# Performance work log

Hardware: AMD Instinct MI355X
Metric: run time of the kernel (lower is better)

Reference implementation:

```python
import jax, jax.numpy as jnp
import numpy as np

D_MODEL = 1024
N_HEADS = 16
HEAD_DIM = D_MODEL // N_HEADS


def setup_inputs() -> dict:
    key = jax.random.key(0)
    k1, k2, k3, k4, k5 = jax.random.split(key, 5)
    B, S = 2, 2048
    x = jax.random.normal(k1, (B, S, D_MODEL), dtype=jnp.float32)
    mask = jnp.ones((B, 1, S), dtype=jnp.int32)
    s1 = 1.0 / np.sqrt(D_MODEL)
    qkv_w = jax.random.normal(k2, (3 * D_MODEL, D_MODEL), dtype=jnp.float32) * s1
    qkv_b = jax.random.normal(k3, (3 * D_MODEL,), dtype=jnp.float32) * 0.02
    wo_w = jax.random.normal(k4, (D_MODEL, D_MODEL), dtype=jnp.float32) * s1
    wo_b = jax.random.normal(k5, (D_MODEL,), dtype=jnp.float32) * 0.02
    return {"x": x, "mask": mask, "qkv_w": qkv_w, "qkv_b": qkv_b, "wo_w": wo_w, "wo_b": wo_b}


def reference(x, mask, qkv_w, qkv_b, wo_w, wo_b):
    B, S, _ = x.shape
    # fused QKV projection: [B,S,3d]
    qkv = jnp.einsum('bsd,ed->bse', x, qkv_w) + qkv_b
    qkv = qkv.reshape(B, S, 3, N_HEADS, HEAD_DIM).transpose(2, 0, 3, 1, 4)
    q, k, v = qkv[0], qkv[1], qkv[2]  # each [B,H,S,hd]
    scores = jnp.einsum('bhsd,bhtd->bhst', q, k) / np.sqrt(HEAD_DIM)
    # mask [B,1,S] -> [B,1,1,S]; fill -inf where mask == 0
    scores = jnp.where(mask[:, None] == 0, -jnp.inf, scores)
    weights = jax.nn.softmax(scores, axis=-1)  # dropout p=0.0 -> identity
    out = jnp.einsum('bhst,bhtd->bhsd', weights, v)
    out = out.transpose(0, 2, 1, 3).reshape(B, S, D_MODEL)
    out = jnp.einsum('bsd,ed->bse', out, wo_w) + wo_b
    return out, weights
```

## Files before the change

### kernel.cpp

```cpp
#include <hip/hip_runtime.h>
#include <cstdint>
#include <cstddef>

typedef unsigned short u16;
typedef __attribute__((ext_vector_type(8))) short bf16x8;
typedef __attribute__((ext_vector_type(4))) float f32x4;

#define DEV static __device__ __forceinline__

DEV void gload_lds16(const void* g, void* l) {
  __builtin_amdgcn_global_load_lds((const __attribute__((address_space(1))) void*)g,
                                   (__attribute__((address_space(3))) void*)l, 16, 0, 0);
}

DEV u16 f2bf(float f) {
  unsigned x = __float_as_uint(f);
  return (u16)((x + 0x7FFFu + ((x >> 16) & 1u)) >> 16);
}

DEV unsigned cvtpk(float lo, float hi) {
  unsigned r;
  asm("v_cvt_pk_bf16_f32 %0, %1, %2" : "=v"(r) : "v"(lo), "v"(hi));
  return r;
}

#if __has_builtin(__builtin_amdgcn_exp2f)
DEV float fexp2(float x) { return __builtin_amdgcn_exp2f(x); }
#else
DEV float fexp2(float x) { return exp2f(x); }
#endif

#define WAITV(n)                                                   \
  do {                                                             \
    asm volatile("s_waitcnt vmcnt(" #n ")" ::: "memory");          \
    __builtin_amdgcn_sched_barrier(0);                             \
  } while (0)

DEV void sbar() {
  __builtin_amdgcn_sched_barrier(0);
  __builtin_amdgcn_s_barrier();
  __builtin_amdgcn_sched_barrier(0);
}

__global__ __launch_bounds__(256) void cvt3(const float* __restrict__ a, u16* __restrict__ da,
                                            const float* __restrict__ b, u16* __restrict__ db,
                                            const float* __restrict__ c, u16* __restrict__ dc) {
  int bid = blockIdx.x;
  const float* s;
  u16* d;
  int base;
  if (bid < 4096) { s = a; d = da; base = bid; }
  else if (bid < 7168) { s = b; d = db; base = bid - 4096; }
  else { s = c; d = dc; base = bid - 7168; }
  const int i = (base * 256 + (int)threadIdx.x) * 4;
  float4 v = *(const float4*)(s + i);
  uint2 p;
  p.x = (unsigned)f2bf(v.x) | ((unsigned)f2bf(v.y) << 16);
  p.y = (unsigned)f2bf(v.z) | ((unsigned)f2bf(v.w) << 16);
  *(uint2*)(d + i) = p;
}

template <int EPI, int BM, int BN>
__global__ __launch_bounds__(256) void gemm_bt(const u16* __restrict__ A,
                                               const u16* __restrict__ Bm,
                                               const float* __restrict__ bias,
                                               void* __restrict__ Cout,
                                               u16* __restrict__ Vt,
                                               int M, int N, int K) {
  __shared__ u16 As[2][BM * 32];
  __shared__ u16 Bs[2][BN * 32];
  constexpr int MT = BM / 32, NT = BN / 32;
  const int cpx = (int)gridDim.x >> 3;
  const int bid = ((int)blockIdx.x & 7) * cpx + ((int)blockIdx.x >> 3);
  const int nb = N / BN;
  const int m0 = (bid / nb) * BM;
  const int n0 = (bid % nb) * BN;
  const int tid = threadIdx.x;
  const int w = tid >> 6, lane = tid & 63;
  const int wm = (w >> 1) * (BM / 2), wn = (w & 1) * (BN / 2);
  const int lr = lane & 15, lg = lane >> 4;

  f32x4 acc[MT][NT];
  const f32x4 z4 = {0.f, 0.f, 0.f, 0.f};
#pragma unroll
  for (int m = 0; m < MT; ++m)
#pragma unroll
    for (int n = 0; n < NT; ++n) acc[m][n] = z4;

  auto stage = [&](int ks, int buf) {
    const int k0 = ks << 5;
#pragma unroll
    for (int i = 0; i < BM * 4 / 256; ++i) {
      const int o = i * 256 + tid;
      const int row = o >> 2, c = o & 3;
      gload_lds16(A + (size_t)(m0 + row) * K + k0 + c * 8, &As[buf][(i * 256 + w * 64) * 8]);
    }
#pragma unroll
    for (int i = 0; i < BN * 4 / 256; ++i) {
      const int o = i * 256 + tid;
      const int row = o >> 2, c = o & 3;
      gload_lds16(Bm + (size_t)(n0 + row) * K + k0 + c * 8, &Bs[buf][(i * 256 + w * 64) * 8]);
    }
  };

  const int nk = K >> 5;
  stage(0, 0);
  __syncthreads();
  for (int ks = 0; ks < nk; ++ks) {
    const int cur = ks & 1;
    if (ks + 1 < nk) stage(ks + 1, cur ^ 1);
    bf16x8 af[MT], bfr[NT];
#pragma unroll
    for (int m = 0; m < MT; ++m)
      af[m] = *(const bf16x8*)&As[cur][(wm + m * 16 + lr) * 32 + lg * 8];
#pragma unroll
    for (int n = 0; n < NT; ++n)
      bfr[n] = *(const bf16x8*)&Bs[cur][(wn + n * 16 + lr) * 32 + lg * 8];
    __builtin_amdgcn_s_setprio(1);
#pragma unroll
    for (int m = 0; m < MT; ++m)
#pragma unroll
      for (int n = 0; n < NT; ++n)
        acc[m][n] = __builtin_amdgcn_mfma_f32_16x16x32_bf16(af[m], bfr[n], acc[m][n], 0, 0, 0);
    __builtin_amdgcn_s_setprio(0);
    __syncthreads();
  }

#pragma unroll
  for (int n = 0; n < NT; ++n) {
    const int e = n0 + wn + n * 16 + lr;
    const float bv = bias[e];
    if (EPI == 1 && (e >> 10) == 2) {
      const int h = (e >> 6) & 15, d = e & 63;
#pragma unroll
      for (int m = 0; m < MT; ++m) {
        const int row0 = m0 + wm + m * 16 + lg * 4;
        const int bb = row0 >> 11, s0 = row0 & 2047;
        uint2 pv;
        pv.x = cvtpk(acc[m][n][0] + bv, acc[m][n][1] + bv);
        pv.y = cvtpk(acc[m][n][2] + bv, acc[m][n][3] + bv);
        *(uint2*)(Vt + (size_t)(bb * 16 + h) * 131072 + (size_t)d * 2048 + s0) = pv;
      }
    } else {
#pragma unroll
      for (int m = 0; m < MT; ++m) {
#pragma unroll
        for (int r = 0; r < 4; ++r) {
          const int row = m0 + wm + m * 16 + lg * 4 + r;
          const float v = acc[m][n][r] + bv;
          if (EPI == 0) {
            ((float*)Cout)[(size_t)row * N + e] = v;
          } else {
            const int which = e >> 10, h = (e >> 6) & 15, d = e & 63;
            const int bb = row >> 11, s = row & 2047;
            ((u16*)Cout)[(size_t)which * 4194304 +
                         (((size_t)(bb * 16 + h) * 2048 + s) << 6) + d] = f2bf(v);
          }
        }
      }
    }
  }
}

__global__ __launch_bounds__(256, 4) void attn(const u16* __restrict__ Q,
                                               const u16* __restrict__ Kg,
                                               const u16* __restrict__ Vtg,
                                               const int* __restrict__ mask,
                                               float* __restrict__ Wout,
                                               u16* __restrict__ Og) {
  __shared__ u16 Ks[2][64 * 64];
  __shared__ u16 Vs[2][64 * 64];
  __shared__ u16 Pl[4][16 * 64];
  const int L = ((int)blockIdx.x & 7) * 128 + ((int)blockIdx.x >> 3);
  const int bh = L >> 5, qt = L & 31;
  const int b = bh >> 4, h = bh & 15;
  const int tid = threadIdx.x;
  const int w = tid >> 6, lane = tid & 63;
  const int lr = lane & 15, lg = lane >> 4;
  const int srow0 = qt * 64 + w * 16;
  const float C2 = 0.18033688011112042f;
  const float M2 = 11.541560327111707f;

  const u16* qrow = Q + ((size_t)bh * 2048 + srow0 + lr) * 64;
  const bf16x8 qf0 = *(const bf16x8*)(qrow + lg * 8);
  const bf16x8 qf1 = *(const bf16x8*)(qrow + 32 + lg * 8);
  const int* mrow = mask + b * 2048;

  auto stageK = [&](int kt, u16* dst) {
    const u16* g = Kg + (size_t)bh * 131072 + (size_t)kt * 4096;
#pragma unroll
    for (int iss = 0; iss < 2; ++iss) {
      const int o = iss * 256 + tid;
      const int row = o >> 3, c = o & 7;
      gload_lds16(g + row * 64 + ((c ^ (row & 7)) << 3), dst + (iss * 256 + w * 64) * 8);
    }
  };
  auto stageV = [&](int kt, u16* dst) {
    const u16* g = Vtg + (size_t)bh * 131072 + kt * 64;
#pragma unroll
    for (int iss = 0; iss < 2; ++iss) {
      const int o = iss * 256 + tid;
      const int row = o >> 3, c = o & 7;
      gload_lds16(g + (size_t)row * 2048 + ((c ^ (row & 7)) << 3),
                  dst + (iss * 256 + w * 64) * 8);
    }
  };
  auto probs = [&](const u16* kb, int kt, f32x4* pr) {
    int4 mv[4];
#pragma unroll
    for (int n = 0; n < 4; ++n) mv[n] = *(const int4*)&mrow[kt * 64 + n * 16 + lg * 4];
    f32x4 sc[4];
    __builtin_amdgcn_s_setprio(1);
#pragma unroll
    for (int n = 0; n < 4; ++n) {
      const int tr = n * 16 + lr;
      const bf16x8 k0 = *(const bf16x8*)&kb[tr * 64 + ((lg ^ (tr & 7)) << 3)];
      const bf16x8 k1 = *(const bf16x8*)&kb[tr * 64 + (((lg + 4) ^ (tr & 7)) << 3)];
      f32x4 s = {0.f, 0.f, 0.f, 0.f};
      s = __builtin_amdgcn_mfma_f32_16x16x32_bf16(k0, qf0, s, 0, 0, 0);
      s = __builtin_amdgcn_mfma_f32_16x16x32_bf16(k1, qf1, s, 0, 0, 0);
      sc[n] = s;
    }
    __builtin_amdgcn_s_setprio(0);
#pragma unroll
    for (int n = 0; n < 4; ++n) {
      f32x4 p;
      p[0] = (mv[n].x == 0) ? 0.f : fexp2(fmaf(sc[n][0], C2, -M2));
      p[1] = (mv[n].y == 0) ? 0.f : fexp2(fmaf(sc[n][1], C2, -M2));
      p[2] = (mv[n].z == 0) ? 0.f : fexp2(fmaf(sc[n][2], C2, -M2));
      p[3] = (mv[n].w == 0) ? 0.f : fexp2(fmaf(sc[n][3], C2, -M2));
      pr[n] = p;
    }
  };

  stageK(0, &Ks[0][0]);
  stageK(1, &Ks[1][0]);
  WAITV(2);
  sbar();
  float lsum = 0.f;
  int cur3 = 0, stg3 = 2;
  for (int t = 0; t < 32; ++t) {
    u16* curb = (cur3 == 0) ? &Ks[0][0] : ((cur3 == 1) ? &Ks[1][0] : &Vs[0][0]);
    if (t + 2 < 32) {
      u16* stb = (stg3 == 0) ? &Ks[0][0] : ((stg3 == 1) ? &Ks[1][0] : &Vs[0][0]);
      stageK(t + 2, stb);
    }
    f32x4 pr[4];
    probs(curb, t, pr);
    float s0 = (pr[0][0] + pr[0][1]) + (pr[0][2] + pr[0][3]);
    float s1 = (pr[1][0] + pr[1][1]) + (pr[1][2] + pr[1][3]);
    float s2 = (pr[2][0] + pr[2][1]) + (pr[2][2] + pr[2][3]);
    float s3 = (pr[3][0] + pr[3][1]) + (pr[3][2] + pr[3][3]);
    lsum += (s0 + s1) + (s2 + s3);
    if (t + 1 < 32) {
      if (t + 2 < 32) {
        WAITV(6);
      } else {
        WAITV(0);
      }
      sbar();
    }
    cur3 = (cur3 == 2) ? 0 : cur3 + 1;
    stg3 = (stg3 == 2) ? 0 : stg3 + 1;
  }
  lsum += __shfl_xor(lsum, 16);
  lsum += __shfl_xor(lsum, 32);
  const float rl = 1.0f / lsum;

  sbar();
  f32x4 oacc[4];
  const f32x4 z4 = {0.f, 0.f, 0.f, 0.f};
#pragma unroll
  for (int n = 0; n < 4; ++n) oacc[n] = z4;

  float* wrow = Wout + ((size_t)bh * 2048 + srow0 + lr) * 2048;
  char* plw = (char*)&Pl[w][0];
  const int pswz = (lr & 7) << 4;

  stageK(0, &Ks[0][0]);
  stageV(0, &Vs[0][0]);
  WAITV(0);
  sbar();
  for (int t = 0; t < 32; ++t) {
    const int cur = t & 1;
    if (t + 1 < 32) {
      stageK(t + 1, &Ks[cur ^ 1][0]);
      stageV(t + 1, &Vs[cur ^ 1][0]);
    }
    f32x4 pr[4];
    probs(&Ks[cur][0], t, pr);
#pragma unroll
    for (int n = 0; n < 4; ++n) {
      f32x4 wv;
      wv[0] = pr[n][0] * rl;
      wv[1] = pr[n][1] * rl;
      wv[2] = pr[n][2] * rl;
      wv[3] = pr[n][3] * rl;
      __builtin_nontemporal_store(wv, (f32x4*)&wrow[t * 64 + n * 16 + lg * 4]);
      uint2 pw;
      pw.x = cvtpk(wv[0], wv[1]);
      pw.y = cvtpk(wv[2], wv[3]);
      *(uint2*)(plw + (lr * 128 + ((n * 32 + lg * 8) ^ pswz))) = pw;
    }
    const bf16x8 pf0 = *(const bf16x8*)(plw + (lr * 128 + ((lg * 16) ^ pswz)));
    const bf16x8 pf1 = *(const bf16x8*)(plw + (lr * 128 + ((64 + lg * 16) ^ pswz)));
    __builtin_amdgcn_s_setprio(1);
#pragma unroll
    for (int n = 0; n < 4; ++n) {
      const int dr = n * 16 + lr;
      const bf16x8 v0 = *(const bf16x8*)&Vs[cur][dr * 64 + ((lg ^ (dr & 7)) << 3)];
      const bf16x8 v1 = *(const bf16x8*)&Vs[cur][dr * 64 + (((lg + 4) ^ (dr & 7)) << 3)];
      oacc[n] = __builtin_amdgcn_mfma_f32_16x16x32_bf16(pf0, v0, oacc[n], 0, 0, 0);
      oacc[n] = __builtin_amdgcn_mfma_f32_16x16x32_bf16(pf1, v1, oacc[n], 0, 0, 0);
    }
    __builtin_amdgcn_s_setprio(0);
    if (t + 1 < 32) {
      WAITV(8);
      sbar();
    }
  }

#pragma unroll
  for (int n = 0; n < 4; ++n) {
#pragma unroll
    for (int r = 0; r < 4; ++r) {
      const int s = srow0 + lg * 4 + r;
      Og[((size_t)(b * 2048 + s)) * 1024 + h * 64 + n * 16 + lr] = f2bf(oacc[n][r]);
    }
  }
}

extern "C" void kernel_launch(void* const* d_in, const int* in_sizes, int n_in,
                              void* d_out, int out_size, void* d_ws, size_t ws_size,
                              hipStream_t stream) {
  const float* x     = (const float*)d_in[0];
  const int*   mask  = (const int*)d_in[1];
  const float* qkv_w = (const float*)d_in[2];
  const float* qkv_b = (const float*)d_in[3];
  const float* wo_w  = (const float*)d_in[4];
  const float* wo_b  = (const float*)d_in[5];
  float* out = (float*)d_out;

  char* ws = (char*)d_ws;
  u16* xb   = (u16*)(ws);
  u16* qwb  = (u16*)(ws + (8u << 20));
  u16* wob  = (u16*)(ws + (14u << 20));
  u16* qkvb = (u16*)(ws + (16u << 20));
  u16* vt   = (u16*)(ws + (40u << 20));
  u16* ob   = (u16*)(ws + (48u << 20));

  cvt3<<<8192, 256, 0, stream>>>(x, xb, qkv_w, qwb, wo_w, wob);
  gemm_bt<1, 128, 128><<<768, 256, 0, stream>>>(xb, qwb, qkv_b, qkvb, vt, 4096, 3072, 1024);
  attn<<<1024, 256, 0, stream>>>(qkvb, qkvb + 4194304, vt, mask, out + 4194304, ob);
  gemm_bt<0, 128, 64><<<512, 256, 0, stream>>>(ob, wob, wo_b, out, nullptr, 4096, 1024, 1024);
}
```

Baseline: 248.2 us.

## Process two query tiles per attention block to reuse K/V LDS tiles

Each attention block now handles 128 query rows: every wave computes two 16-row query subtiles against each staged K/V tile, so K and V are loaded into LDS half as often. The first pass stages 128-row K chunks in one larger double buffer. The grid is halved, launch bounds go to 2 blocks per CU, and the wait counts are adjusted for the extra loads. The cost is higher register pressure and fewer resident blocks. The kernel is likely dominated by writing the large fp32 weights output, so the reuse gain may be small.

```diff
diff --git a/kernel.cpp b/kernel.cpp
--- a/kernel.cpp
+++ b/kernel.cpp
@@ -162,30 +162,41 @@
   }
 }
 
-__global__ __launch_bounds__(256, 4) void attn(const u16* __restrict__ Q,
+__global__ __launch_bounds__(256, 2) void attn(const u16* __restrict__ Q,
                                                const u16* __restrict__ Kg,
                                                const u16* __restrict__ Vtg,
                                                const int* __restrict__ mask,
                                                float* __restrict__ Wout,
                                                u16* __restrict__ Og) {
-  __shared__ u16 Ks[2][64 * 64];
-  __shared__ u16 Vs[2][64 * 64];
-  __shared__ u16 Pl[4][16 * 64];
-  const int L = ((int)blockIdx.x & 7) * 128 + ((int)blockIdx.x >> 3);
-  const int bh = L >> 5, qt = L & 31;
+  __shared__ u16 SM[2][8192];
+  __shared__ u16 Pl[4][2][1024];
+  const int L = ((int)blockIdx.x & 7) * 64 + ((int)blockIdx.x >> 3);
+  const int bh = L >> 4, qt = L & 15;
   const int b = bh >> 4, h = bh & 15;
   const int tid = threadIdx.x;
   const int w = tid >> 6, lane = tid & 63;
   const int lr = lane & 15, lg = lane >> 4;
-  const int srow0 = qt * 64 + w * 16;
+  const int srow0 = qt * 128 + w * 16;
   const float C2 = 0.18033688011112042f;
   const float M2 = 11.541560327111707f;
 
-  const u16* qrow = Q + ((size_t)bh * 2048 + srow0 + lr) * 64;
-  const bf16x8 qf0 = *(const bf16x8*)(qrow + lg * 8);
-  const bf16x8 qf1 = *(const bf16x8*)(qrow + 32 + lg * 8);
+  const u16* qr0 = Q + ((size_t)bh * 2048 + srow0 + lr) * 64;
+  const u16* qr1 = qr0 + 64 * 64;
+  const bf16x8 qf00 = *(const bf16x8*)(qr0 + lg * 8);
+  const bf16x8 qf01 = *(const bf16x8*)(qr0 + 32 + lg * 8);
+  const bf16x8 qf10 = *(const bf16x8*)(qr1 + lg * 8);
+  const bf16x8 qf11 = *(const bf16x8*)(qr1 + 32 + lg * 8);
   const int* mrow = mask + b * 2048;
 
+  auto stageChunk = [&](int ch, u16* dst) {
+    const u16* g = Kg + (size_t)bh * 131072 + (size_t)ch * 8192;
+#pragma unroll
+    for (int iss = 0; iss < 4; ++iss) {
+      const int o = iss * 256 + tid;
+      const int row = o >> 3, c = o & 7;
+      gload_lds16(g + row * 64 + ((c ^ (row & 7)) << 3), dst + (iss * 256 + w * 64) * 8);
+    }
+  };
   auto stageK = [&](int kt, u16* dst) {
     const u16* g = Kg + (size_t)bh * 131072 + (size_t)kt * 4096;
 #pragma unroll
@@ -205,129 +216,166 @@
                   dst + (iss * 256 + w * 64) * 8);
     }
   };
-  auto probs = [&](const u16* kb, int kt, f32x4* pr) {
+  auto probsT = [&](const u16* kb, int tt, int kt, f32x4 pr[2][4]) {
     int4 mv[4];
 #pragma unroll
     for (int n = 0; n < 4; ++n) mv[n] = *(const int4*)&mrow[kt * 64 + n * 16 + lg * 4];
-    f32x4 sc[4];
-    __builtin_amdgcn_s_setprio(1);
+    bf16x8 k0[4], k1[4];
 #pragma unroll
     for (int n = 0; n < 4; ++n) {
       const int tr = n * 16 + lr;
-      const bf16x8 k0 = *(const bf16x8*)&kb[tr * 64 + ((lg ^ (tr & 7)) << 3)];
-      const bf16x8 k1 = *(const bf16x8*)&kb[tr * 64 + (((lg + 4) ^ (tr & 7)) << 3)];
+      k0[n] = *(const bf16x8*)&kb[tt + tr * 64 + ((lg ^ (tr & 7)) << 3)];
+      k1[n] = *(const bf16x8*)&kb[tt + tr * 64 + (((lg + 4) ^ (tr & 7)) << 3)];
+    }
+    f32x4 sc[2][4];
+    __builtin_amdgcn_s_setprio(1);
+#pragma unroll
+    for (int n = 0; n < 4; ++n) {
       f32x4 s = {0.f, 0.f, 0.f, 0.f};
-      s = __builtin_amdgcn_mfma_f32_16x16x32_bf16(k0, qf0, s, 0, 0, 0);
-      s = __builtin_amdgcn_mfma_f32_16x16x32_bf16(k1, qf1, s, 0, 0, 0);
-      sc[n] = s;
+      s = __builtin_amdgcn_mfma_f32_16x16x32_bf16(k0[n], qf00, s, 0, 0, 0);
+      s = __builtin_amdgcn_mfma_f32_16x16x32_bf16(k1[n], qf01, s, 0, 0, 0);
+      sc[0][n] = s;
+      f32x4 s2 = {0.f, 0.f, 0.f, 0.f};
+      s2 = __builtin_amdgcn_mfma_f32_16x16x32_bf16(k0[n], qf10, s2, 0, 0, 0);
+      s2 = __builtin_amdgcn_mfma_f32_16x16x32_bf16(k1[n], qf11, s2, 0, 0, 0);
+      sc[1][n] = s2;
     }
     __builtin_amdgcn_s_setprio(0);
 #pragma unroll
-    for (int n = 0; n < 4; ++n) {
-      f32x4 p;
-      p[0] = (mv[n].x == 0) ? 0.f : fexp2(fmaf(sc[n][0], C2, -M2));
-      p[1] = (mv[n].y == 0) ? 0.f : fexp2(fmaf(sc[n][1], C2, -M2));
-      p[2] = (mv[n].z == 0) ? 0.f : fexp2(fmaf(sc[n][2], C2, -M2));
-      p[3] = (mv[n].w == 0) ? 0.f : fexp2(fmaf(sc[n][3], C2, -M2));
-      pr[n] = p;
-    }
+    for (int hh = 0; hh < 2; ++hh)
+#pragma unroll
+      for (int n = 0; n < 4; ++n) {
+        f32x4 p;
+        p[0] = (mv[n].x == 0) ? 0.f : fexp2(fmaf(sc[hh][n][0], C2, -M2));
+        p[1] = (mv[n].y == 0) ? 0.f : fexp2(fmaf(sc[hh][n][1], C2, -M2));
+        p[2] = (mv[n].z == 0) ? 0.f : fexp2(fmaf(sc[hh][n][2], C2, -M2));
+        p[3] = (mv[n].w == 0) ? 0.f : fexp2(fmaf(sc[hh][n][3], C2, -M2));
+        pr[hh][n] = p;
+      }
   };
 
-  stageK(0, &Ks[0][0]);
-  stageK(1, &Ks[1][0]);
-  WAITV(2);
+  float ls0 = 0.f, ls1 = 0.f;
+  stageChunk(0, &SM[0][0]);
+  WAITV(0);
   sbar();
-  float lsum = 0.f;
-  int cur3 = 0, stg3 = 2;
-  for (int t = 0; t < 32; ++t) {
-    u16* curb = (cur3 == 0) ? &Ks[0][0] : ((cur3 == 1) ? &Ks[1][0] : &Vs[0][0]);
-    if (t + 2 < 32) {
-      u16* stb = (stg3 == 0) ? &Ks[0][0] : ((stg3 == 1) ? &Ks[1][0] : &Vs[0][0]);
-      stageK(t + 2, stb);
-    }
-    f32x4 pr[4];
-    probs(curb, t, pr);
-    float s0 = (pr[0][0] + pr[0][1]) + (pr[0][2] + pr[0][3]);
-    float s1 = (pr[1][0] + pr[1][1]) + (pr[1][2] + pr[1][3]);
-    float s2 = (pr[2][0] + pr[2][1]) + (pr[2][2] + pr[2][3]);
-    float s3 = (pr[3][0] + pr[3][1]) + (pr[3][2] + pr[3][3]);
-    lsum += (s0 + s1) + (s2 + s3);
-    if (t + 1 < 32) {
-      if (t + 2 < 32) {
-        WAITV(6);
-      } else {
-        WAITV(0);
-      }
+  for (int r = 0; r < 16; ++r) {
+    const u16* cb = &SM[r & 1][0];
+    if (r + 1 < 16) stageChunk(r + 1, &SM[(r + 1) & 1][0]);
+#pragma unroll
+    for (int half = 0; half < 2; ++half) {
+      f32x4 pr[2][4];
+      probsT(cb, half * 4096, 2 * r + half, pr);
+      {
+        float s0 = (pr[0][0][0] + pr[0][0][1]) + (pr[0][0][2] + pr[0][0][3]);
+        float s1 = (pr[0][1][0] + pr[0][1][1]) + (pr[0][1][2] + pr[0][1][3]);
+        float s2 = (pr[0][2][0] + pr[0][2][1]) + (pr[0][2][2] + pr[0][2][3]);
+        float s3 = (pr[0][3][0] + pr[0][3][1]) + (pr[0][3][2] + pr[0][3][3]);
+        ls0 += (s0 + s1) + (s2 + s3);
+      }
+      {
+        float s0 = (pr[1][0][0] + pr[1][0][1]) + (pr[1][0][2] + pr[1][0][3]);
+        float s1 = (pr[1][1][0] + pr[1][1][1]) + (pr[1][1][2] + pr[1][1][3]);
+        float s2 = (pr[1][2][0] + pr[1][2][1]) + (pr[1][2][2] + pr[1][2][3]);
+        float s3 = (pr[1][3][0] + pr[1][3][1]) + (pr[1][3][2] + pr[1][3][3]);
+        ls1 += (s0 + s1) + (s2 + s3);
+      }
+    }
+    if (r + 1 < 16) {
+      WAITV(8);
       sbar();
     }
-    cur3 = (cur3 == 2) ? 0 : cur3 + 1;
-    stg3 = (stg3 == 2) ? 0 : stg3 + 1;
   }
-  lsum += __shfl_xor(lsum, 16);
-  lsum += __shfl_xor(lsum, 32);
-  const float rl = 1.0f / lsum;
+  ls0 += __shfl_xor(ls0, 16);
+  ls0 += __shfl_xor(ls0, 32);
+  ls1 += __shfl_xor(ls1, 16);
+  ls1 += __shfl_xor(ls1, 32);
+  const float rl0 = 1.0f / ls0, rl1 = 1.0f / ls1;
 
   sbar();
-  f32x4 oacc[4];
+  f32x4 oacc[2][4];
   const f32x4 z4 = {0.f, 0.f, 0.f, 0.f};
 #pragma unroll
-  for (int n = 0; n < 4; ++n) oacc[n] = z4;
-
-  float* wrow = Wout + ((size_t)bh * 2048 + srow0 + lr) * 2048;
-  char* plw = (char*)&Pl[w][0];
+  for (int hh = 0; hh < 2; ++hh)
+#pragma unroll
+    for (int n = 0; n < 4; ++n) oacc[hh][n] = z4;
+
+  float* wrow0 = Wout + ((size_t)bh * 2048 + srow0 + lr) * 2048;
+  float* wrow1 = wrow0 + (size_t)64 * 2048;
+  char* plw0 = (char*)&Pl[w][0][0];
+  char* plw1 = (char*)&Pl[w][1][0];
   const int pswz = (lr & 7) << 4;
 
-  stageK(0, &Ks[0][0]);
-  stageV(0, &Vs[0][0]);
+  stageK(0, &SM[0][0]);
+  stageV(0, &SM[1][0]);
   WAITV(0);
   sbar();
   for (int t = 0; t < 32; ++t) {
     const int cur = t & 1;
+    u16* kcur = &SM[0][cur * 4096];
+    u16* vcur = &SM[1][cur * 4096];
     if (t + 1 < 32) {
-      stageK(t + 1, &Ks[cur ^ 1][0]);
-      stageV(t + 1, &Vs[cur ^ 1][0]);
-    }
-    f32x4 pr[4];
-    probs(&Ks[cur][0], t, pr);
+      stageK(t + 1, &SM[0][(cur ^ 1) * 4096]);
+      stageV(t + 1, &SM[1][(cur ^ 1) * 4096]);
+    }
+    f32x4 pr[2][4];
+    probsT(kcur, 0, t, pr);
 #pragma unroll
     for (int n = 0; n < 4; ++n) {
       f32x4 wv;
-      wv[0] = pr[n][0] * rl;
-      wv[1] = pr[n][1] * rl;
-      wv[2] = pr[n][2] * rl;
-      wv[3] = pr[n][3] * rl;
-      __builtin_nontemporal_store(wv, (f32x4*)&wrow[t * 64 + n * 16 + lg * 4]);
+      wv[0] = pr[0][n][0] * rl0;
+      wv[1] = pr[0][n][1] * rl0;
+      wv[2] = pr[0][n][2] * rl0;
+      wv[3] = pr[0][n][3] * rl0;
+      __builtin_nontemporal_store(wv, (f32x4*)&wrow0[t * 64 + n * 16 + lg * 4]);
       uint2 pw;
       pw.x = cvtpk(wv[0], wv[1]);
       pw.y = cvtpk(wv[2], wv[3]);
-      *(uint2*)(plw + (lr * 128 + ((n * 32 + lg * 8) ^ pswz))) = pw;
-    }
-    const bf16x8 pf0 = *(const bf16x8*)(plw + (lr * 128 + ((lg * 16) ^ pswz)));
-    const bf16x8 pf1 = *(const bf16x8*)(plw + (lr * 128 + ((64 + lg * 16) ^ pswz)));
+      *(uint2*)(plw0 + (lr * 128 + ((n * 32 + lg * 8) ^ pswz))) = pw;
+    }
+#pragma unroll
+    for (int n = 0; n < 4; ++n) {
+      f32x4 wv;
+      wv[0] = pr[1][n][0] * rl1;
+      wv[1] = pr[1][n][1] * rl1;
+      wv[2] = pr[1][n][2] * rl1;
+      wv[3] = pr[1][n][3] * rl1;
+      __builtin_nontemporal_store(wv, (f32x4*)&wrow1[t * 64 + n * 16 + lg * 4]);
+      uint2 pw;
+      pw.x = cvtpk(wv[0], wv[1]);
+      pw.y = cvtpk(wv[2], wv[3]);
+      *(uint2*)(plw1 + (lr * 128 + ((n * 32 + lg * 8) ^ pswz))) = pw;
+    }
+    const bf16x8 pA0 = *(const bf16x8*)(plw0 + (lr * 128 + ((lg * 16) ^ pswz)));
+    const bf16x8 pA1 = *(const bf16x8*)(plw0 + (lr * 128 + ((64 + lg * 16) ^ pswz)));
+    const bf16x8 pB0 = *(const bf16x8*)(plw1 + (lr * 128 + ((lg * 16) ^ pswz)));
+    const bf16x8 pB1 = *(const bf16x8*)(plw1 + (lr * 128 + ((64 + lg * 16) ^ pswz)));
     __builtin_amdgcn_s_setprio(1);
 #pragma unroll
     for (int n = 0; n < 4; ++n) {
       const int dr = n * 16 + lr;
-      const bf16x8 v0 = *(const bf16x8*)&Vs[cur][dr * 64 + ((lg ^ (dr & 7)) << 3)];
-      const bf16x8 v1 = *(const bf16x8*)&Vs[cur][dr * 64 + (((lg + 4) ^ (dr & 7)) << 3)];
-      oacc[n] = __builtin_amdgcn_mfma_f32_16x16x32_bf16(pf0, v0, oacc[n], 0, 0, 0);
-      oacc[n] = __builtin_amdgcn_mfma_f32_16x16x32_bf16(pf1, v1, oacc[n], 0, 0, 0);
+      const bf16x8 v0 = *(const bf16x8*)&vcur[dr * 64 + ((lg ^ (dr & 7)) << 3)];
+      const bf16x8 v1 = *(const bf16x8*)&vcur[dr * 64 + (((lg + 4) ^ (dr & 7)) << 3)];
+      oacc[0][n] = __builtin_amdgcn_mfma_f32_16x16x32_bf16(pA0, v0, oacc[0][n], 0, 0, 0);
+      oacc[0][n] = __builtin_amdgcn_mfma_f32_16x16x32_bf16(pA1, v1, oacc[0][n], 0, 0, 0);
+      oacc[1][n] = __builtin_amdgcn_mfma_f32_16x16x32_bf16(pB0, v0, oacc[1][n], 0, 0, 0);
+      oacc[1][n] = __builtin_amdgcn_mfma_f32_16x16x32_bf16(pB1, v1, oacc[1][n], 0, 0, 0);
     }
     __builtin_amdgcn_s_setprio(0);
     if (t + 1 < 32) {
-      WAITV(8);
+      WAITV(12);
       sbar();
     }
   }
 
 #pragma unroll
-  for (int n = 0; n < 4; ++n) {
-#pragma unroll
-    for (int r = 0; r < 4; ++r) {
-      const int s = srow0 + lg * 4 + r;
-      Og[((size_t)(b * 2048 + s)) * 1024 + h * 64 + n * 16 + lr] = f2bf(oacc[n][r]);
-    }
-  }
+  for (int hh = 0; hh < 2; ++hh)
+#pragma unroll
+    for (int n = 0; n < 4; ++n)
+#pragma unroll
+      for (int r = 0; r < 4; ++r) {
+        const int s = srow0 + hh * 64 + lg * 4 + r;
+        Og[((size_t)(b * 2048 + s)) * 1024 + h * 64 + n * 16 + lr] = f2bf(oacc[hh][n][r]);
+      }
 }
 
 extern "C" void kernel_launch(void* const* d_in, const int* in_sizes, int n_in,
@@ -351,6 +399,6 @@
 
   cvt3<<<8192, 256, 0, stream>>>(x, xb, qkv_w, qwb, wo_w, wob);
   gemm_bt<1, 128, 128><<<768, 256, 0, stream>>>(xb, qwb, qkv_b, qkvb, vt, 4096, 3072, 1024);
-  attn<<<1024, 256, 0, stream>>>(qkvb, qkvb + 4194304, vt, mask, out + 4194304, ob);
+  attn<<<512, 256, 0, stream>>>(qkvb, qkvb + 4194304, vt, mask, out + 4194304, ob);
   gemm_bt<0, 128, 64><<<512, 256, 0, stream>>>(ob, wob, wo_b, out, nullptr, 4096, 1024, 1024);
 }
```

Result: slower. 276.6 us (+11.4%).

## Bit-pack mask and restage attention weights through LDS for coalesced stores

Applied to the files above, without the earlier changes.

The attention kernel now stages the normalized fp32 probabilities through a swizzled LDS tile per wave. Each group of 8 lanes then writes one contiguous 128-byte row segment of the large weights output, instead of 16-byte pieces scattered across 16 rows. The same LDS readback builds the bf16 P fragment for the PV MFMA, split into two K halves. The int32 mask is pre-packed into bitwords by an extra block in the conversion kernel. An all-ones check skips the per-element select work. The cost is extra LDS traffic and instructions per tile, plus a workspace region for the packed mask placed inside the qkv buffer area.

```diff
diff --git a/kernel.cpp b/kernel.cpp
--- a/kernel.cpp
+++ b/kernel.cpp
@@ -44,8 +44,20 @@
 
 __global__ __launch_bounds__(256) void cvt3(const float* __restrict__ a, u16* __restrict__ da,
                                             const float* __restrict__ b, u16* __restrict__ db,
-                                            const float* __restrict__ c, u16* __restrict__ dc) {
+                                            const float* __restrict__ c, u16* __restrict__ dc,
+                                            const int* __restrict__ mask,
+                                            unsigned* __restrict__ mpack) {
   int bid = blockIdx.x;
+  if (bid == 8192) {
+    const int j = threadIdx.x;
+    if (j < 128) {
+      const int* mb = mask + (j >> 6) * 2048 + (j & 63) * 32;
+      unsigned bits = 0;
+      for (int k = 0; k < 32; ++k) bits |= (mb[k] != 0 ? 1u : 0u) << k;
+      mpack[j] = bits;
+    }
+    return;
+  }
   const float* s;
   u16* d;
   int base;
@@ -165,12 +177,12 @@
 __global__ __launch_bounds__(256, 4) void attn(const u16* __restrict__ Q,
                                                const u16* __restrict__ Kg,
                                                const u16* __restrict__ Vtg,
-                                               const int* __restrict__ mask,
+                                               const unsigned* __restrict__ mpack,
                                                float* __restrict__ Wout,
                                                u16* __restrict__ Og) {
-  __shared__ u16 Ks[2][64 * 64];
-  __shared__ u16 Vs[2][64 * 64];
-  __shared__ u16 Pl[4][16 * 64];
+  __shared__ u16 Ks[2][4096];
+  __shared__ u16 Vs[2][4096];
+  __shared__ float Pf[4][512];
   const int L = ((int)blockIdx.x & 7) * 128 + ((int)blockIdx.x >> 3);
   const int bh = L >> 5, qt = L & 31;
   const int b = bh >> 4, h = bh & 15;
@@ -184,7 +196,7 @@
   const u16* qrow = Q + ((size_t)bh * 2048 + srow0 + lr) * 64;
   const bf16x8 qf0 = *(const bf16x8*)(qrow + lg * 8);
   const bf16x8 qf1 = *(const bf16x8*)(qrow + 32 + lg * 8);
-  const int* mrow = mask + b * 2048;
+  const unsigned* mpk = mpack + b * 64;
 
   auto stageK = [&](int kt, u16* dst) {
     const u16* g = Kg + (size_t)bh * 131072 + (size_t)kt * 4096;
@@ -205,32 +217,20 @@
                   dst + (iss * 256 + w * 64) * 8);
     }
   };
-  auto probs = [&](const u16* kb, int kt, f32x4* pr) {
-    int4 mv[4];
-#pragma unroll
-    for (int n = 0; n < 4; ++n) mv[n] = *(const int4*)&mrow[kt * 64 + n * 16 + lg * 4];
-    f32x4 sc[4];
+  auto qk = [&](const u16* kb, f32x4* sc) {
+    const f32x4 z4 = {0.f, 0.f, 0.f, 0.f};
     __builtin_amdgcn_s_setprio(1);
 #pragma unroll
     for (int n = 0; n < 4; ++n) {
       const int tr = n * 16 + lr;
       const bf16x8 k0 = *(const bf16x8*)&kb[tr * 64 + ((lg ^ (tr & 7)) << 3)];
       const bf16x8 k1 = *(const bf16x8*)&kb[tr * 64 + (((lg + 4) ^ (tr & 7)) << 3)];
-      f32x4 s = {0.f, 0.f, 0.f, 0.f};
+      f32x4 s = z4;
       s = __builtin_amdgcn_mfma_f32_16x16x32_bf16(k0, qf0, s, 0, 0, 0);
       s = __builtin_amdgcn_mfma_f32_16x16x32_bf16(k1, qf1, s, 0, 0, 0);
       sc[n] = s;
     }
     __builtin_amdgcn_s_setprio(0);
-#pragma unroll
-    for (int n = 0; n < 4; ++n) {
-      f32x4 p;
-      p[0] = (mv[n].x == 0) ? 0.f : fexp2(fmaf(sc[n][0], C2, -M2));
-      p[1] = (mv[n].y == 0) ? 0.f : fexp2(fmaf(sc[n][1], C2, -M2));
-      p[2] = (mv[n].z == 0) ? 0.f : fexp2(fmaf(sc[n][2], C2, -M2));
-      p[3] = (mv[n].w == 0) ? 0.f : fexp2(fmaf(sc[n][3], C2, -M2));
-      pr[n] = p;
-    }
   };
 
   stageK(0, &Ks[0][0]);
@@ -241,20 +241,34 @@
   int cur3 = 0, stg3 = 2;
   for (int t = 0; t < 32; ++t) {
     u16* curb = (cur3 == 0) ? &Ks[0][0] : ((cur3 == 1) ? &Ks[1][0] : &Vs[0][0]);
+    const unsigned mx = mpk[t * 2], my = mpk[t * 2 + 1];
     if (t + 2 < 32) {
       u16* stb = (stg3 == 0) ? &Ks[0][0] : ((stg3 == 1) ? &Ks[1][0] : &Vs[0][0]);
       stageK(t + 2, stb);
     }
-    f32x4 pr[4];
-    probs(curb, t, pr);
-    float s0 = (pr[0][0] + pr[0][1]) + (pr[0][2] + pr[0][3]);
-    float s1 = (pr[1][0] + pr[1][1]) + (pr[1][2] + pr[1][3]);
-    float s2 = (pr[2][0] + pr[2][1]) + (pr[2][2] + pr[2][3]);
-    float s3 = (pr[3][0] + pr[3][1]) + (pr[3][2] + pr[3][3]);
-    lsum += (s0 + s1) + (s2 + s3);
+    f32x4 sc[4];
+    qk(curb, sc);
+    f32x4 p[4];
+#pragma unroll
+    for (int n = 0; n < 4; ++n)
+#pragma unroll
+      for (int r = 0; r < 4; ++r) p[n][r] = fexp2(fmaf(sc[n][r], C2, -M2));
+    if ((mx & my) != 0xFFFFFFFFu) {
+#pragma unroll
+      for (int n = 0; n < 4; ++n) {
+        const unsigned wsel = (n < 2) ? mx : my;
+#pragma unroll
+        for (int r = 0; r < 4; ++r) {
+          const unsigned bit = (wsel >> ((n & 1) * 16 + lg * 4 + r)) & 1u;
+          p[n][r] = bit ? p[n][r] : 0.f;
+        }
+      }
+    }
+#pragma unroll
+    for (int n = 0; n < 4; ++n) lsum += (p[n][0] + p[n][1]) + (p[n][2] + p[n][3]);
     if (t + 1 < 32) {
       if (t + 2 < 32) {
-        WAITV(6);
+        WAITV(2);
       } else {
         WAITV(0);
       }
@@ -273,9 +287,10 @@
 #pragma unroll
   for (int n = 0; n < 4; ++n) oacc[n] = z4;
 
-  float* wrow = Wout + ((size_t)bh * 2048 + srow0 + lr) * 2048;
-  char* plw = (char*)&Pl[w][0];
-  const int pswz = (lr & 7) << 4;
+  float* Wb = Wout + (size_t)bh * 2048 * 2048;
+  char* pfw = (char*)&Pf[w][0];
+  const int sw = (lr & 7) << 4;
+  const int ql0 = lane >> 3, ch = lane & 7;
 
   stageK(0, &Ks[0][0]);
   stageV(0, &Vs[0][0]);
@@ -283,51 +298,70 @@
   sbar();
   for (int t = 0; t < 32; ++t) {
     const int cur = t & 1;
+    const unsigned mx = mpk[t * 2], my = mpk[t * 2 + 1];
     if (t + 1 < 32) {
       stageK(t + 1, &Ks[cur ^ 1][0]);
       stageV(t + 1, &Vs[cur ^ 1][0]);
     }
-    f32x4 pr[4];
-    probs(&Ks[cur][0], t, pr);
-#pragma unroll
-    for (int n = 0; n < 4; ++n) {
-      f32x4 wv;
-      wv[0] = pr[n][0] * rl;
-      wv[1] = pr[n][1] * rl;
-      wv[2] = pr[n][2] * rl;
-      wv[3] = pr[n][3] * rl;
-      __builtin_nontemporal_store(wv, (f32x4*)&wrow[t * 64 + n * 16 + lg * 4]);
-      uint2 pw;
-      pw.x = cvtpk(wv[0], wv[1]);
-      pw.y = cvtpk(wv[2], wv[3]);
-      *(uint2*)(plw + (lr * 128 + ((n * 32 + lg * 8) ^ pswz))) = pw;
-    }
-    const bf16x8 pf0 = *(const bf16x8*)(plw + (lr * 128 + ((lg * 16) ^ pswz)));
-    const bf16x8 pf1 = *(const bf16x8*)(plw + (lr * 128 + ((64 + lg * 16) ^ pswz)));
-    __builtin_amdgcn_s_setprio(1);
-#pragma unroll
-    for (int n = 0; n < 4; ++n) {
-      const int dr = n * 16 + lr;
-      const bf16x8 v0 = *(const bf16x8*)&Vs[cur][dr * 64 + ((lg ^ (dr & 7)) << 3)];
-      const bf16x8 v1 = *(const bf16x8*)&Vs[cur][dr * 64 + (((lg + 4) ^ (dr & 7)) << 3)];
-      oacc[n] = __builtin_amdgcn_mfma_f32_16x16x32_bf16(pf0, v0, oacc[n], 0, 0, 0);
-      oacc[n] = __builtin_amdgcn_mfma_f32_16x16x32_bf16(pf1, v1, oacc[n], 0, 0, 0);
-    }
-    __builtin_amdgcn_s_setprio(0);
+    f32x4 sc[4];
+    qk(&Ks[cur][0], sc);
+    f32x4 wv[4];
+#pragma unroll
+    for (int n = 0; n < 4; ++n)
+#pragma unroll
+      for (int r = 0; r < 4; ++r) wv[n][r] = fexp2(fmaf(sc[n][r], C2, -M2)) * rl;
+    if ((mx & my) != 0xFFFFFFFFu) {
+#pragma unroll
+      for (int n = 0; n < 4; ++n) {
+        const unsigned wsel = (n < 2) ? mx : my;
+#pragma unroll
+        for (int r = 0; r < 4; ++r) {
+          const unsigned bit = (wsel >> ((n & 1) * 16 + lg * 4 + r)) & 1u;
+          wv[n][r] = bit ? wv[n][r] : 0.f;
+        }
+      }
+    }
+#pragma unroll
+    for (int hh = 0; hh < 2; ++hh) {
+      *(f32x4*)(pfw + (lr * 128 + ((lg * 16) ^ sw))) = wv[2 * hh];
+      *(f32x4*)(pfw + (lr * 128 + ((64 + lg * 16) ^ sw))) = wv[2 * hh + 1];
+#pragma unroll
+      for (int s2 = 0; s2 < 2; ++s2) {
+        const int ql = s2 * 8 + ql0;
+        const f32x4 rv = *(const f32x4*)(pfw + (ql * 128 + ((ch * 16) ^ ((ql & 7) << 4))));
+        __builtin_nontemporal_store(
+            rv, (f32x4*)(Wb + (size_t)(srow0 + ql) * 2048 + t * 64 + hh * 32 + ch * 4));
+      }
+      const f32x4 a0 = *(const f32x4*)(pfw + (lr * 128 + ((lg * 32) ^ sw)));
+      const f32x4 a1 = *(const f32x4*)(pfw + (lr * 128 + ((lg * 32 + 16) ^ sw)));
+      int4 pk4;
+      pk4.x = cvtpk(a0[0], a0[1]);
+      pk4.y = cvtpk(a0[2], a0[3]);
+      pk4.z = cvtpk(a1[0], a1[1]);
+      pk4.w = cvtpk(a1[2], a1[3]);
+      const bf16x8 pfr = *(const bf16x8*)&pk4;
+      __builtin_amdgcn_s_setprio(1);
+#pragma unroll
+      for (int n = 0; n < 4; ++n) {
+        const int dr = n * 16 + lr;
+        const bf16x8 vf = *(const bf16x8*)&Vs[cur][dr * 64 + (((lg + hh * 4) ^ (dr & 7)) << 3)];
+        oacc[n] = __builtin_amdgcn_mfma_f32_16x16x32_bf16(pfr, vf, oacc[n], 0, 0, 0);
+      }
+      __builtin_amdgcn_s_setprio(0);
+    }
     if (t + 1 < 32) {
-      WAITV(8);
+      WAITV(4);
       sbar();
     }
   }
 
 #pragma unroll
-  for (int n = 0; n < 4; ++n) {
+  for (int n = 0; n < 4; ++n)
 #pragma unroll
     for (int r = 0; r < 4; ++r) {
       const int s = srow0 + lg * 4 + r;
       Og[((size_t)(b * 2048 + s)) * 1024 + h * 64 + n * 16 + lr] = f2bf(oacc[n][r]);
     }
-  }
 }
 
 extern "C" void kernel_launch(void* const* d_in, const int* in_sizes, int n_in,
@@ -346,11 +380,12 @@
   u16* qwb  = (u16*)(ws + (8u << 20));
   u16* wob  = (u16*)(ws + (14u << 20));
   u16* qkvb = (u16*)(ws + (16u << 20));
+  unsigned* mpack = (unsigned*)(ws + (16u << 20) + 16777216);
   u16* vt   = (u16*)(ws + (40u << 20));
   u16* ob   = (u16*)(ws + (48u << 20));
 
-  cvt3<<<8192, 256, 0, stream>>>(x, xb, qkv_w, qwb, wo_w, wob);
+  cvt3<<<8193, 256, 0, stream>>>(x, xb, qkv_w, qwb, wo_w, wob, mask, mpack);
   gemm_bt<1, 128, 128><<<768, 256, 0, stream>>>(xb, qwb, qkv_b, qkvb, vt, 4096, 3072, 1024);
-  attn<<<1024, 256, 0, stream>>>(qkvb, qkvb + 4194304, vt, mask, out + 4194304, ob);
+  attn<<<1024, 256, 0, stream>>>(qkvb, qkvb + 4194304, vt, mpack, out + 4194304, ob);
   gemm_bt<0, 128, 64><<<512, 256, 0, stream>>>(ob, wob, wo_b, out, nullptr, 4096, 1024, 1024);
 }
```

New measurement: 201.6 us. 18.8% less time.
